# Performance work log

Hardware: AMD Instinct MI355X
Metric: run time of the kernel (lower is better)

Reference implementation:

```python
import jax, jax.numpy as jnp
import numpy as np

CH = 512
NUM_HEADS = 8
NUM_GROUPS = 32  # min(32, channels)
EPS = 1e-5


def setup_inputs() -> dict:
    key = jax.random.key(0)
    ks = jax.random.split(key, 4)
    B, C, H, W = 8, CH, 32, 32
    x = jax.random.normal(ks[0], (B, C, H, W), dtype=jnp.float32)
    gn_weight = jnp.ones((C,), dtype=jnp.float32)
    gn_bias = jnp.zeros((C,), dtype=jnp.float32)
    # 1x1 conv weights stored as [out_ch, in_ch] (kernel dims squeezed)
    qkv_weight = jax.random.normal(ks[1], (3 * C, C), dtype=jnp.float32) * (C ** -0.5)
    qkv_bias = jnp.zeros((3 * C,), dtype=jnp.float32)
    proj_weight = jax.random.normal(ks[2], (C, C), dtype=jnp.float32) * (C ** -0.5)
    proj_bias = jnp.zeros((C,), dtype=jnp.float32)
    return {
        "x": x,
        "gn_weight": gn_weight,
        "gn_bias": gn_bias,
        "qkv_weight": qkv_weight,
        "qkv_bias": qkv_bias,
        "proj_weight": proj_weight,
        "proj_bias": proj_bias,
    }


def _group_norm(x, weight, bias):
    B, C, H, W = x.shape
    g = x.reshape(B, NUM_GROUPS, C // NUM_GROUPS, H, W)
    mean = jnp.mean(g, axis=(2, 3, 4), keepdims=True)
    var = jnp.var(g, axis=(2, 3, 4), keepdims=True)
    g = (g - mean) * jax.lax.rsqrt(var + EPS)
    g = g.reshape(B, C, H, W)
    return g * weight[None, :, None, None] + bias[None, :, None, None]


def reference(x, gn_weight, gn_bias, qkv_weight, qkv_bias, proj_weight, proj_bias):
    B, C, H, W = x.shape
    nh = NUM_HEADS
    hc = C // nh
    N = H * W

    h = _group_norm(x, gn_weight, gn_bias)
    # 1x1 conv == per-pixel matmul
    qkv = jnp.einsum('oc,bchw->bohw', qkv_weight, h) + qkv_bias[None, :, None, None]
    q, k, v = jnp.split(qkv, 3, axis=1)
    # b (h c) x y -> b h c (x y)
    q = q.reshape(B, nh, hc, N)
    k = k.reshape(B, nh, hc, N)
    v = v.reshape(B, nh, hc, N)

    scale = hc ** -0.5
    attn = jnp.einsum('bhci,bhcj->bhij', q, k) * scale  # [B, nh, N, N]
    attn = jax.nn.softmax(attn, axis=-1)
    out = jnp.einsum('bhij,bhcj->bhci', attn, v)  # [B, nh, hc, N]
    out = out.reshape(B, C, H, W)
    out = jnp.einsum('oc,bchw->bohw', proj_weight, out) + proj_bias[None, :, None, None]
    return x + out
```

## Files before the change

### kernel.cpp

```cpp
#include <hip/hip_runtime.h>
#include <math.h>

#define B_   8
#define C_   512
#define N_   1024
#define NH_  8
#define HC_  64

typedef __attribute__((ext_vector_type(8))) short bf16x8;
typedef __attribute__((ext_vector_type(4))) float f32x4;

#define MFMA16(a, b, c) __builtin_amdgcn_mfma_f32_16x16x32_bf16(a, b, c, 0, 0, 0)

__device__ __forceinline__ unsigned short f2bf(float f) {
  unsigned u = __builtin_bit_cast(unsigned, f);
  u += 0x7fffu + ((u >> 16) & 1u);
  return (unsigned short)(u >> 16);
}

__device__ __forceinline__ unsigned short f2bf_trunc(float f) {
  return (unsigned short)(__builtin_bit_cast(unsigned, f) >> 16);
}

__device__ __forceinline__ unsigned pack2(float a, float b) {
  return (unsigned)f2bf(a) | ((unsigned)f2bf(b) << 16);
}

__device__ __forceinline__ void gll16(const void* g, void* l) {
  __builtin_amdgcn_global_load_lds(
      (const __attribute__((address_space(1))) unsigned int*)g,
      (__attribute__((address_space(3))) unsigned int*)l, 16, 0, 0);
}

__global__ __launch_bounds__(256) void prep(const float* __restrict__ x,
                                            const float* __restrict__ gw,
                                            const float* __restrict__ gb,
                                            const float* __restrict__ qkvw,
                                            const float* __restrict__ pw,
                                            unsigned short* __restrict__ hT,
                                            unsigned short* __restrict__ qkvw_bf,
                                            unsigned short* __restrict__ projw_bf) {
  const int t = threadIdx.x;
  if (blockIdx.x >= 256) {
    const int widx = blockIdx.x - 256;
    const float* src = (widx < 768) ? qkvw : pw;
    unsigned short* dst = (widx < 768) ? qkvw_bf : projw_bf;
    const int i = ((widx < 768) ? widx : widx - 768) * 1024 + t * 4;
    const float4 v = *(const float4*)(src + i);
    ushort4 o;
    o.x = f2bf(v.x); o.y = f2bf(v.y); o.z = f2bf(v.z); o.w = f2bf(v.w);
    *(ushort4*)(dst + i) = o;
    return;
  }
  const int b = blockIdx.x >> 5;
  const int g = blockIdx.x & 31;
  const float* xg = x + ((size_t)b * C_ + (size_t)g * 16) * N_;

  float4 xv[16];
  float s = 0.f, ss = 0.f;
#pragma unroll
  for (int k = 0; k < 16; ++k) {
    xv[k] = *(const float4*)(xg + (size_t)k * N_ + t * 4);
    s  += xv[k].x + xv[k].y + xv[k].z + xv[k].w;
    ss += xv[k].x * xv[k].x + xv[k].y * xv[k].y + xv[k].z * xv[k].z + xv[k].w * xv[k].w;
  }
#pragma unroll
  for (int off = 32; off > 0; off >>= 1) {
    s  += __shfl_down(s, off);
    ss += __shfl_down(ss, off);
  }
  __shared__ float rs[4], rss[4], sh_mi[2];
  if ((t & 63) == 0) { rs[t >> 6] = s; rss[t >> 6] = ss; }
  __syncthreads();
  if (t == 0) {
    s  = rs[0] + rs[1] + rs[2] + rs[3];
    ss = rss[0] + rss[1] + rss[2] + rss[3];
    const float mean = s * (1.f / 16384.f);
    const float var  = ss * (1.f / 16384.f) - mean * mean;
    sh_mi[0] = mean;
    sh_mi[1] = rsqrtf(var + 1e-5f);
  }
  __syncthreads();
  const float mean = sh_mi[0], inv = sh_mi[1];

  float sc[16], of[16];
#pragma unroll
  for (int k = 0; k < 16; ++k) {
    const int c = g * 16 + k;
    sc[k] = inv * gw[c];
    of[k] = gb[c] - mean * sc[k];
  }
#pragma unroll
  for (int r = 0; r < 4; ++r) {
    const int p = t * 4 + r;
    unsigned short* dst = hT + ((size_t)b * N_ + p) * C_ + g * 16;
    uint4 o0, o1;
#pragma unroll
    for (int k2 = 0; k2 < 4; ++k2) {
      const float a0 = ((const float*)&xv[k2 * 2 + 0])[r] * sc[k2 * 2 + 0] + of[k2 * 2 + 0];
      const float a1 = ((const float*)&xv[k2 * 2 + 1])[r] * sc[k2 * 2 + 1] + of[k2 * 2 + 1];
      ((unsigned*)&o0)[k2] = pack2(a0, a1);
      const float b0 = ((const float*)&xv[8 + k2 * 2 + 0])[r] * sc[8 + k2 * 2 + 0] + of[8 + k2 * 2 + 0];
      const float b1 = ((const float*)&xv[8 + k2 * 2 + 1])[r] * sc[8 + k2 * 2 + 1] + of[8 + k2 * 2 + 1];
      ((unsigned*)&o1)[k2] = pack2(b0, b1);
    }
    *(uint4*)(dst)     = o0;
    *(uint4*)(dst + 8) = o1;
  }
}

__global__ __launch_bounds__(256, 3) void gemm_qkv(
    const unsigned short* __restrict__ A, const float* __restrict__ bias,
    const unsigned short* __restrict__ BT, unsigned short* __restrict__ qkTout,
    unsigned short* __restrict__ vout) {
  __shared__ __attribute__((aligned(16))) short lds[128 * 136];
  const int t = threadIdx.x;
  const int lane = t & 63, w = t >> 6;
  const int lm = lane & 15, q = lane >> 4;
  const int wm = w >> 1, wn = w & 1;
  const int b = blockIdx.z;
  const int m0 = blockIdx.y * 128, n0 = blockIdx.x * 128;
  const unsigned short* Bb = BT + (size_t)b * N_ * C_;

  f32x4 acc[4][4];
#pragma unroll
  for (int i = 0; i < 4; ++i)
#pragma unroll
    for (int j = 0; j < 4; ++j) acc[i][j] = (f32x4){0.f, 0.f, 0.f, 0.f};

  for (int k0 = 0; k0 < C_; k0 += 64) {
    __syncthreads();
#pragma unroll
    for (int rr = 0; rr < 2; ++rr) {
      const int rg = w * 2 + rr;
#pragma unroll
      for (int ks = 0; ks < 2; ++ks) {
        gll16(A  + (size_t)(m0 + rg * 16 + lm) * C_ + k0 + ks * 32 + q * 8,
              lds + (rg * 2 + ks) * 512);
        gll16(Bb + (size_t)(n0 + rg * 16 + lm) * C_ + k0 + ks * 32 + q * 8,
              lds + (16 + rg * 2 + ks) * 512);
      }
    }
    __syncthreads();
    bf16x8 af[4][2];
#pragma unroll
    for (int mi = 0; mi < 4; ++mi)
#pragma unroll
      for (int ks = 0; ks < 2; ++ks)
        af[mi][ks] = *(const bf16x8*)(lds + (((wm * 4 + mi) * 2) + ks) * 512 + lane * 8);
#pragma unroll
    for (int ni = 0; ni < 4; ++ni)
#pragma unroll
      for (int ks = 0; ks < 2; ++ks) {
        const bf16x8 bfr =
            *(const bf16x8*)(lds + (16 + ((wn * 4 + ni) * 2) + ks) * 512 + lane * 8);
#pragma unroll
        for (int mi = 0; mi < 4; ++mi)
          acc[mi][ni] = MFMA16(af[mi][ks], bfr, acc[mi][ni]);
      }
  }

  __syncthreads();
  if (blockIdx.y < 8) {
    const float qs = (blockIdx.y < 4) ? 0.125f : 1.0f;
#pragma unroll
    for (int mi = 0; mi < 4; ++mi) {
#pragma unroll
      for (int ni = 0; ni < 4; ++ni) {
        const int pl = wn * 64 + ni * 16 + lm;
        const int ol0 = wm * 64 + mi * 16 + q * 4;
        ushort4 o4;
        o4.x = f2bf((acc[mi][ni][0] + bias[m0 + ol0 + 0]) * qs);
        o4.y = f2bf((acc[mi][ni][1] + bias[m0 + ol0 + 1]) * qs);
        o4.z = f2bf((acc[mi][ni][2] + bias[m0 + ol0 + 2]) * qs);
        o4.w = f2bf((acc[mi][ni][3] + bias[m0 + ol0 + 3]) * qs);
        *(ushort4*)&lds[pl * 136 + ol0] = o4;
      }
    }
    __syncthreads();
#pragma unroll
    for (int u = 0; u < 8; ++u) {
      const int flat = u * 256 + t;
      const int oc = flat & 15, pl = flat >> 4;
      *(uint4*)&qkTout[((size_t)b * N_ + n0 + pl) * 1024 + m0 + oc * 8] =
          *(const uint4*)&lds[pl * 136 + oc * 8];
    }
  } else {
#pragma unroll
    for (int mi = 0; mi < 4; ++mi)
#pragma unroll
      for (int ni = 0; ni < 4; ++ni) {
        const int pl = wn * 64 + ni * 16 + lm;
#pragma unroll
        for (int r = 0; r < 4; ++r) {
          const int ol = wm * 64 + mi * 16 + q * 4 + r;
          lds[ol * 136 + pl] = f2bf(acc[mi][ni][r] + bias[m0 + ol]);
        }
      }
    __syncthreads();
    const int c0 = m0 - 1024;
#pragma unroll
    for (int u = 0; u < 8; ++u) {
      const int flat = u * 256 + t;
      const int pc = flat & 15, ol = flat >> 4;
      *(uint4*)&vout[((size_t)b * 512 + c0 + ol) * N_ + n0 + pc * 8] =
          *(const uint4*)&lds[ol * 136 + pc * 8];
    }
  }
}

__global__ __launch_bounds__(256, 2) void gemm_proj(
    const unsigned short* __restrict__ A, const float* __restrict__ bias,
    const unsigned short* __restrict__ BT, const float* __restrict__ resid,
    float* __restrict__ outf) {
  __shared__ __attribute__((aligned(16))) short lds[24 * 512];
  const int t = threadIdx.x;
  const int lane = t & 63, w = t >> 6;
  const int lm = lane & 15, q = lane >> 4;
  const int wm = w >> 1, wn = w & 1;
  const int b = blockIdx.z;
  const int m0 = blockIdx.y * 128, n0 = blockIdx.x * 64;
  const unsigned short* Bb = BT + (size_t)b * N_ * C_;

  f32x4 acc[4][2];
#pragma unroll
  for (int i = 0; i < 4; ++i)
#pragma unroll
    for (int j = 0; j < 2; ++j) acc[i][j] = (f32x4){0.f, 0.f, 0.f, 0.f};

  for (int k0 = 0; k0 < C_; k0 += 64) {
    __syncthreads();
#pragma unroll
    for (int rr = 0; rr < 2; ++rr) {
      const int rg = w * 2 + rr;
#pragma unroll
      for (int ks = 0; ks < 2; ++ks)
        gll16(A + (size_t)(m0 + rg * 16 + lm) * C_ + k0 + ks * 32 + q * 8,
              lds + (rg * 2 + ks) * 512);
    }
#pragma unroll
    for (int ks = 0; ks < 2; ++ks)
      gll16(Bb + (size_t)(n0 + w * 16 + lm) * C_ + k0 + ks * 32 + q * 8,
            lds + (16 + w * 2 + ks) * 512);
    __syncthreads();
    bf16x8 af[4][2];
#pragma unroll
    for (int mi = 0; mi < 4; ++mi)
#pragma unroll
      for (int ks = 0; ks < 2; ++ks)
        af[mi][ks] = *(const bf16x8*)(lds + (((wm * 4 + mi) * 2) + ks) * 512 + lane * 8);
#pragma unroll
    for (int ni = 0; ni < 2; ++ni)
#pragma unroll
      for (int ks = 0; ks < 2; ++ks) {
        const bf16x8 bfr =
            *(const bf16x8*)(lds + (16 + ((wn * 2 + ni) * 2) + ks) * 512 + lane * 8);
#pragma unroll
        for (int mi = 0; mi < 4; ++mi)
          acc[mi][ni] = MFMA16(af[mi][ks], bfr, acc[mi][ni]);
      }
  }

#pragma unroll
  for (int mi = 0; mi < 4; ++mi)
#pragma unroll
    for (int ni = 0; ni < 2; ++ni) {
      const int col = n0 + wn * 32 + ni * 16 + lm;
#pragma unroll
      for (int r = 0; r < 4; ++r) {
        const int row = m0 + wm * 64 + mi * 16 + q * 4 + r;
        const size_t oi = ((size_t)b * 512 + row) * N_ + col;
        outf[oi] = acc[mi][ni][r] + bias[row] + resid[oi];
      }
    }
}

__global__ __launch_bounds__(256, 4) void attn_mfma(
    const unsigned short* __restrict__ qkT, const unsigned short* __restrict__ vbuf,
    unsigned short* __restrict__ aoT) {
  __shared__ __attribute__((aligned(16))) short lds[32 * 512];
  short* Qb = lds;
  short* Kb = lds + 8 * 512;
  short* Vb = lds + 16 * 512;
  short* Pb = lds + 24 * 512;

  const int t = threadIdx.x;
  const int lane = t & 63, w = t >> 6;
  const int lm = lane & 15, q = lane >> 4;
  const int i0 = blockIdx.x * 64;
  const int hh = blockIdx.y;
  const int b = blockIdx.z;

  const unsigned short* QT = qkT + (size_t)b * N_ * 1024;
  const unsigned short* Vp = vbuf + ((size_t)b * 512 + hh * 64) * N_;

#pragma unroll
  for (int ff = 0; ff < 2; ++ff)
    gll16(QT + (size_t)(i0 + w * 16 + lm) * 1024 + hh * 64 + ff * 32 + q * 8,
          Qb + (w * 2 + ff) * 512);
  __syncthreads();

  bf16x8 af[2];
#pragma unroll
  for (int ks = 0; ks < 2; ++ks)
    af[ks] = *(const bf16x8*)(Qb + (w * 2 + ks) * 512 + lane * 8);

  f32x4 accO[4], lrun = (f32x4){0.f, 0.f, 0.f, 0.f};
#pragma unroll
  for (int nc = 0; nc < 4; ++nc) accO[nc] = (f32x4){0.f, 0.f, 0.f, 0.f};

  for (int jt = 0; jt < 16; ++jt) {
    const int j0 = jt * 64;
    __syncthreads();
#pragma unroll
    for (int ks = 0; ks < 2; ++ks) {
      gll16(QT + (size_t)(j0 + w * 16 + lm) * 1024 + 512 + hh * 64 + ks * 32 + q * 8,
            Kb + (w * 2 + ks) * 512);
      gll16(Vp + (size_t)(w * 16 + lm) * N_ + j0 + ks * 32 + q * 8,
            Vb + (w * 2 + ks) * 512);
    }
    __syncthreads();

    f32x4 accS[4];
#pragma unroll
    for (int nj = 0; nj < 4; ++nj) accS[nj] = (f32x4){0.f, 0.f, 0.f, 0.f};
#pragma unroll
    for (int nj = 0; nj < 4; ++nj)
#pragma unroll
      for (int ks = 0; ks < 2; ++ks) {
        const bf16x8 bfr = *(const bf16x8*)(Kb + (nj * 2 + ks) * 512 + lane * 8);
        accS[nj] = MFMA16(af[ks], bfr, accS[nj]);
      }

#pragma unroll
    for (int nj = 0; nj < 4; ++nj)
#pragma unroll
      for (int r = 0; r < 4; ++r) {
        const float p = __expf(accS[nj][r]);
        accS[nj][r] = p;
        lrun[r] += p;
      }
#pragma unroll
    for (int nj = 0; nj < 4; ++nj) {
      const int jin = nj * 16 + lm;
      const int ks = jin >> 5;
      const int qt = (jin >> 3) & 3;
      const int jp = jin & 7;
      short* pp = Pb + (w * 2 + ks) * 512 + qt * 128 + jp;
#pragma unroll
      for (int r = 0; r < 4; ++r)
        pp[(q * 4 + r) * 8] = (short)f2bf_trunc(accS[nj][r]);
    }

#pragma unroll
    for (int ks = 0; ks < 2; ++ks) {
      const bf16x8 pf = *(const bf16x8*)(Pb + (w * 2 + ks) * 512 + lane * 8);
#pragma unroll
      for (int nc = 0; nc < 4; ++nc) {
        const bf16x8 vf = *(const bf16x8*)(Vb + (nc * 2 + ks) * 512 + lane * 8);
        accO[nc] = MFMA16(pf, vf, accO[nc]);
      }
    }
  }

#pragma unroll
  for (int d = 1; d <= 8; d <<= 1)
#pragma unroll
    for (int r = 0; r < 4; ++r) lrun[r] += __shfl_xor(lrun[r], d);
  f32x4 linv;
#pragma unroll
  for (int r = 0; r < 4; ++r) linv[r] = 1.f / lrun[r];

  __syncthreads();
  short* Ep = lds + w * 1152;
#pragma unroll
  for (int nc = 0; nc < 4; ++nc)
#pragma unroll
    for (int r = 0; r < 4; ++r)
      Ep[(q * 4 + r) * 72 + nc * 16 + lm] = f2bf(accO[nc][r] * linv[r]);
  unsigned short* aob = aoT + (size_t)b * N_ * C_;
#pragma unroll
  for (int u = 0; u < 2; ++u) {
    const int flat = u * 64 + lane;
    const int c8 = flat & 7, i = flat >> 3;
    *(uint4*)&aob[(size_t)(i0 + w * 16 + i) * C_ + hh * 64 + c8 * 8] =
        *(const uint4*)&Ep[i * 72 + c8 * 8];
  }
}

extern "C" void kernel_launch(void* const* d_in, const int* in_sizes, int n_in,
                              void* d_out, int out_size, void* d_ws, size_t ws_size,
                              hipStream_t stream) {
  const float* x    = (const float*)d_in[0];
  const float* gw   = (const float*)d_in[1];
  const float* gb   = (const float*)d_in[2];
  const float* qkvw = (const float*)d_in[3];
  const float* qkvb = (const float*)d_in[4];
  const float* pw   = (const float*)d_in[5];
  const float* pb   = (const float*)d_in[6];
  float* out = (float*)d_out;

  unsigned short* hT       = (unsigned short*)d_ws;
  unsigned short* qkvw_bf  = hT + (size_t)B_ * N_ * C_;
  unsigned short* projw_bf = qkvw_bf + 1536 * 512;
  unsigned short* qkT      = projw_bf + 512 * 512;
  unsigned short* vbuf     = qkT + (size_t)B_ * N_ * 1024;
  unsigned short* aoTp     = vbuf + (size_t)B_ * 512 * N_;

  prep<<<1280, 256, 0, stream>>>(x, gw, gb, qkvw, pw, hT, qkvw_bf, projw_bf);
  gemm_qkv<<<dim3(8, 12, B_), 256, 0, stream>>>(qkvw_bf, qkvb, hT, qkT, vbuf);
  attn_mfma<<<dim3(16, NH_, B_), 256, 0, stream>>>(qkT, vbuf, aoTp);
  gemm_proj<<<dim3(16, 4, B_), 256, 0, stream>>>(projw_bf, pb, aoTp, x, out);
}
```

Measured before the change: 165.7 us.

## Enlarge attention key tile, remap blocks per XCD, shrink proj GEMM tile

The attention kernel now processes 128 keys per iteration, halving the number of barriers and load phases. Q fragments are loaded directly from global memory instead of being staged through LDS. The grid is remapped to 1D so that blocks sharing a batch/head land on the same XCD for L2 reuse. The projection GEMM uses 64x64 tiles with more blocks and higher occupancy, which may cost some data reuse; the attention kernel's larger LDS footprint lowers its occupancy.

```diff
diff --git a/kernel.cpp b/kernel.cpp
--- a/kernel.cpp
+++ b/kernel.cpp
@@ -209,155 +209,148 @@
   }
 }
 
-__global__ __launch_bounds__(256, 2) void gemm_proj(
+__global__ __launch_bounds__(256, 4) void gemm_proj(
     const unsigned short* __restrict__ A, const float* __restrict__ bias,
     const unsigned short* __restrict__ BT, const float* __restrict__ resid,
     float* __restrict__ outf) {
-  __shared__ __attribute__((aligned(16))) short lds[24 * 512];
+  __shared__ __attribute__((aligned(16))) short lds[16 * 512];
   const int t = threadIdx.x;
   const int lane = t & 63, w = t >> 6;
   const int lm = lane & 15, q = lane >> 4;
   const int wm = w >> 1, wn = w & 1;
   const int b = blockIdx.z;
-  const int m0 = blockIdx.y * 128, n0 = blockIdx.x * 64;
+  const int m0 = blockIdx.y * 64, n0 = blockIdx.x * 64;
   const unsigned short* Bb = BT + (size_t)b * N_ * C_;
 
-  f32x4 acc[4][2];
-#pragma unroll
-  for (int i = 0; i < 4; ++i)
+  f32x4 acc[2][2];
+#pragma unroll
+  for (int i = 0; i < 2; ++i)
 #pragma unroll
     for (int j = 0; j < 2; ++j) acc[i][j] = (f32x4){0.f, 0.f, 0.f, 0.f};
 
   for (int k0 = 0; k0 < C_; k0 += 64) {
     __syncthreads();
 #pragma unroll
-    for (int rr = 0; rr < 2; ++rr) {
-      const int rg = w * 2 + rr;
-#pragma unroll
-      for (int ks = 0; ks < 2; ++ks)
-        gll16(A + (size_t)(m0 + rg * 16 + lm) * C_ + k0 + ks * 32 + q * 8,
-              lds + (rg * 2 + ks) * 512);
-    }
-#pragma unroll
-    for (int ks = 0; ks < 2; ++ks)
+    for (int ks = 0; ks < 2; ++ks) {
+      gll16(A  + (size_t)(m0 + w * 16 + lm) * C_ + k0 + ks * 32 + q * 8,
+            lds + (w * 2 + ks) * 512);
       gll16(Bb + (size_t)(n0 + w * 16 + lm) * C_ + k0 + ks * 32 + q * 8,
-            lds + (16 + w * 2 + ks) * 512);
-    __syncthreads();
-    bf16x8 af[4][2];
-#pragma unroll
-    for (int mi = 0; mi < 4; ++mi)
-#pragma unroll
-      for (int ks = 0; ks < 2; ++ks)
-        af[mi][ks] = *(const bf16x8*)(lds + (((wm * 4 + mi) * 2) + ks) * 512 + lane * 8);
-#pragma unroll
-    for (int ni = 0; ni < 2; ++ni)
-#pragma unroll
-      for (int ks = 0; ks < 2; ++ks) {
+            lds + (8 + w * 2 + ks) * 512);
+    }
+    __syncthreads();
+#pragma unroll
+    for (int ks = 0; ks < 2; ++ks) {
+      bf16x8 af[2];
+#pragma unroll
+      for (int mi = 0; mi < 2; ++mi)
+        af[mi] = *(const bf16x8*)(lds + ((wm * 2 + mi) * 2 + ks) * 512 + lane * 8);
+#pragma unroll
+      for (int ni = 0; ni < 2; ++ni) {
         const bf16x8 bfr =
-            *(const bf16x8*)(lds + (16 + ((wn * 2 + ni) * 2) + ks) * 512 + lane * 8);
-#pragma unroll
-        for (int mi = 0; mi < 4; ++mi)
-          acc[mi][ni] = MFMA16(af[mi][ks], bfr, acc[mi][ni]);
-      }
-  }
-
-#pragma unroll
-  for (int mi = 0; mi < 4; ++mi)
+            *(const bf16x8*)(lds + (8 + (wn * 2 + ni) * 2 + ks) * 512 + lane * 8);
+#pragma unroll
+        for (int mi = 0; mi < 2; ++mi)
+          acc[mi][ni] = MFMA16(af[mi], bfr, acc[mi][ni]);
+      }
+    }
+  }
+
+#pragma unroll
+  for (int mi = 0; mi < 2; ++mi)
 #pragma unroll
     for (int ni = 0; ni < 2; ++ni) {
       const int col = n0 + wn * 32 + ni * 16 + lm;
 #pragma unroll
       for (int r = 0; r < 4; ++r) {
-        const int row = m0 + wm * 64 + mi * 16 + q * 4 + r;
+        const int row = m0 + wm * 32 + mi * 16 + q * 4 + r;
         const size_t oi = ((size_t)b * 512 + row) * N_ + col;
         outf[oi] = acc[mi][ni][r] + bias[row] + resid[oi];
       }
     }
 }
 
-__global__ __launch_bounds__(256, 4) void attn_mfma(
+__global__ __launch_bounds__(256, 3) void attn_mfma(
     const unsigned short* __restrict__ qkT, const unsigned short* __restrict__ vbuf,
     unsigned short* __restrict__ aoT) {
-  __shared__ __attribute__((aligned(16))) short lds[32 * 512];
-  short* Qb = lds;
-  short* Kb = lds + 8 * 512;
-  short* Vb = lds + 16 * 512;
-  short* Pb = lds + 24 * 512;
+  __shared__ __attribute__((aligned(16))) short lds[48 * 512];
+  short* Ks = lds;
+  short* Vs = lds + 16 * 512;
+  short* Pb = lds + 32 * 512;
 
   const int t = threadIdx.x;
   const int lane = t & 63, w = t >> 6;
   const int lm = lane & 15, q = lane >> 4;
-  const int i0 = blockIdx.x * 64;
-  const int hh = blockIdx.y;
-  const int b = blockIdx.z;
+  const int id = blockIdx.x;
+  const int xcd = id & 7, slot = id >> 3;
+  const int pair = xcd * 8 + (slot >> 4);
+  const int b = pair >> 3, hh = pair & 7;
+  const int i0 = (slot & 15) * 64;
 
   const unsigned short* QT = qkT + (size_t)b * N_ * 1024;
   const unsigned short* Vp = vbuf + ((size_t)b * 512 + hh * 64) * N_;
 
-#pragma unroll
-  for (int ff = 0; ff < 2; ++ff)
-    gll16(QT + (size_t)(i0 + w * 16 + lm) * 1024 + hh * 64 + ff * 32 + q * 8,
-          Qb + (w * 2 + ff) * 512);
-  __syncthreads();
-
   bf16x8 af[2];
 #pragma unroll
   for (int ks = 0; ks < 2; ++ks)
-    af[ks] = *(const bf16x8*)(Qb + (w * 2 + ks) * 512 + lane * 8);
+    af[ks] = *(const bf16x8*)(QT + (size_t)(i0 + w * 16 + lm) * 1024 +
+                              hh * 64 + ks * 32 + q * 8);
 
   f32x4 accO[4], lrun = (f32x4){0.f, 0.f, 0.f, 0.f};
 #pragma unroll
   for (int nc = 0; nc < 4; ++nc) accO[nc] = (f32x4){0.f, 0.f, 0.f, 0.f};
 
-  for (int jt = 0; jt < 16; ++jt) {
-    const int j0 = jt * 64;
-    __syncthreads();
-#pragma unroll
-    for (int ks = 0; ks < 2; ++ks) {
-      gll16(QT + (size_t)(j0 + w * 16 + lm) * 1024 + 512 + hh * 64 + ks * 32 + q * 8,
-            Kb + (w * 2 + ks) * 512);
-      gll16(Vp + (size_t)(w * 16 + lm) * N_ + j0 + ks * 32 + q * 8,
-            Vb + (w * 2 + ks) * 512);
-    }
-    __syncthreads();
-
-    f32x4 accS[4];
-#pragma unroll
-    for (int nj = 0; nj < 4; ++nj) accS[nj] = (f32x4){0.f, 0.f, 0.f, 0.f};
-#pragma unroll
-    for (int nj = 0; nj < 4; ++nj)
+  for (int jt = 0; jt < 8; ++jt) {
+    const int j0 = jt * 128;
+    __syncthreads();
+#pragma unroll
+    for (int rr = 0; rr < 2; ++rr) {
+      const int nj = w * 2 + rr;
+#pragma unroll
+      for (int ks = 0; ks < 2; ++ks)
+        gll16(QT + (size_t)(j0 + nj * 16 + lm) * 1024 + 512 + hh * 64 + ks * 32 + q * 8,
+              Ks + (nj * 2 + ks) * 512);
+    }
+#pragma unroll
+    for (int ks2 = 0; ks2 < 4; ++ks2)
+      gll16(Vp + (size_t)(w * 16 + lm) * N_ + j0 + ks2 * 32 + q * 8,
+            Vs + (w * 4 + ks2) * 512);
+    __syncthreads();
+
+    f32x4 accS[8];
+#pragma unroll
+    for (int nj = 0; nj < 8; ++nj) accS[nj] = (f32x4){0.f, 0.f, 0.f, 0.f};
+#pragma unroll
+    for (int nj = 0; nj < 8; ++nj)
 #pragma unroll
       for (int ks = 0; ks < 2; ++ks) {
-        const bf16x8 bfr = *(const bf16x8*)(Kb + (nj * 2 + ks) * 512 + lane * 8);
+        const bf16x8 bfr = *(const bf16x8*)(Ks + (nj * 2 + ks) * 512 + lane * 8);
         accS[nj] = MFMA16(af[ks], bfr, accS[nj]);
       }
 
 #pragma unroll
-    for (int nj = 0; nj < 4; ++nj)
+    for (int nj = 0; nj < 8; ++nj) {
 #pragma unroll
       for (int r = 0; r < 4; ++r) {
         const float p = __expf(accS[nj][r]);
         accS[nj][r] = p;
         lrun[r] += p;
       }
-#pragma unroll
-    for (int nj = 0; nj < 4; ++nj) {
       const int jin = nj * 16 + lm;
-      const int ks = jin >> 5;
-      const int qt = (jin >> 3) & 3;
-      const int jp = jin & 7;
-      short* pp = Pb + (w * 2 + ks) * 512 + qt * 128 + jp;
+      const int ks2 = jin >> 5;
+      const int qt2 = (jin >> 3) & 3;
+      const int jp  = jin & 7;
+      short* pp = Pb + (w * 4 + ks2) * 512 + qt2 * 128 + jp;
 #pragma unroll
       for (int r = 0; r < 4; ++r)
         pp[(q * 4 + r) * 8] = (short)f2bf_trunc(accS[nj][r]);
     }
 
 #pragma unroll
-    for (int ks = 0; ks < 2; ++ks) {
-      const bf16x8 pf = *(const bf16x8*)(Pb + (w * 2 + ks) * 512 + lane * 8);
+    for (int ks2 = 0; ks2 < 4; ++ks2) {
+      const bf16x8 pf = *(const bf16x8*)(Pb + (w * 4 + ks2) * 512 + lane * 8);
 #pragma unroll
       for (int nc = 0; nc < 4; ++nc) {
-        const bf16x8 vf = *(const bf16x8*)(Vb + (nc * 2 + ks) * 512 + lane * 8);
+        const bf16x8 vf = *(const bf16x8*)(Vs + (nc * 4 + ks2) * 512 + lane * 8);
         accO[nc] = MFMA16(pf, vf, accO[nc]);
       }
     }
@@ -409,6 +402,6 @@
 
   prep<<<1280, 256, 0, stream>>>(x, gw, gb, qkvw, pw, hT, qkvw_bf, projw_bf);
   gemm_qkv<<<dim3(8, 12, B_), 256, 0, stream>>>(qkvw_bf, qkvb, hT, qkT, vbuf);
-  attn_mfma<<<dim3(16, NH_, B_), 256, 0, stream>>>(qkT, vbuf, aoTp);
-  gemm_proj<<<dim3(16, 4, B_), 256, 0, stream>>>(projw_bf, pb, aoTp, x, out);
-}
+  attn_mfma<<<1024, 256, 0, stream>>>(qkT, vbuf, aoTp);
+  gemm_proj<<<dim3(16, 8, B_), 256, 0, stream>>>(projw_bf, pb, aoTp, x, out);
+}
```

Measured after the change: 176.6 us. 1.07x slower.
